# Kernel tuning notes

Measured on AMD Instinct MI355X. Metric: run time of the kernel, lower is better.

Reference implementation:

```python
import jax, jax.numpy as jnp
import numpy as np

HEADS = 16
DIM = 1024
D_K = DIM // HEADS
SEQ = 2048


def setup_inputs() -> dict:
    key = jax.random.key(0)
    ks = jax.random.split(key, 11)
    s = 1.0 / np.sqrt(DIM).astype(np.float32)
    return {
        "q": jax.random.normal(ks[0], (SEQ, DIM), jnp.float32),
        "k": jax.random.normal(ks[1], (SEQ, DIM), jnp.float32),
        "v": jax.random.normal(ks[2], (SEQ, DIM), jnp.float32),
        "Wq": jax.random.normal(ks[3], (DIM, DIM), jnp.float32) * s,
        "bq": jax.random.normal(ks[4], (DIM,), jnp.float32) * 0.01,
        "Wk": jax.random.normal(ks[5], (DIM, DIM), jnp.float32) * s,
        "bk": jax.random.normal(ks[6], (DIM,), jnp.float32) * 0.01,
        "Wv": jax.random.normal(ks[7], (DIM, DIM), jnp.float32) * s,
        "bv": jax.random.normal(ks[8], (DIM,), jnp.float32) * 0.01,
        "Wo": jax.random.normal(ks[9], (DIM, DIM), jnp.float32) * s,
        "bo": jax.random.normal(ks[10], (DIM,), jnp.float32) * 0.01,
    }


def reference(q, k, v, Wq, bq, Wk, bk, Wv, bv, Wo, bo):
    S = q.shape[0]
    # torch Linear: x @ W.T + b; view to (1, S, H, d_k) then transpose to (1, H, S, d_k)
    def proj(x, W, b):
        return (x @ W.T + b).reshape(1, S, HEADS, D_K).transpose(0, 2, 1, 3)

    qh = proj(q, Wq, bq)  # (1, H, S, d)
    kh = proj(k, Wk, bk)
    vh = proj(v, Wv, bv)

    scale = 1.0 / np.sqrt(D_K).astype(np.float32)
    scores = jnp.einsum("bhqd,bhkd->bhqk", qh, kh) * scale  # (1, H, S, S)
    # NOTE: source applies softmax over dim=1 == the HEADS axis (faithful quirk)
    attn = jax.nn.softmax(scores, axis=1)
    ctx = jnp.einsum("bhqk,bhkd->bhqd", attn, vh)  # (1, H, S, d)
    concat = ctx.transpose(0, 2, 1, 3).reshape(1, S, DIM)
    return concat @ Wo.T + bo
```

## Files before the change

kernel.cpp:

```cpp
#include <hip/hip_runtime.h>
#include <hip/hip_fp16.h>


typedef _Float16 f16;
typedef _Float16 f16x4 __attribute__((ext_vector_type(4)));
typedef _Float16 f16x8 __attribute__((ext_vector_type(8)));
typedef float    f32x4 __attribute__((ext_vector_type(4)));

#define S_LEN 2048
#define DIM   1024
#define NH    16
#define DK    64
#define EXP2K 0.1803368801111244f

#define MFMA(a, b, c) __builtin_amdgcn_mfma_f32_16x16x32_f16(a, b, c, 0, 0, 0)

#define VM_WAIT0   asm volatile("s_waitcnt vmcnt(0)" ::: "memory")
#define WG_BARRIER asm volatile("s_barrier" ::: "memory")

typedef __attribute__((address_space(1))) void g_void;
typedef __attribute__((address_space(3))) void l_void;

static __device__ __forceinline__ void gload_lds16(const void* g, void* l) {
  __builtin_amdgcn_global_load_lds((g_void*)g, (l_void*)l, 16, 0, 0);
}

static __device__ __forceinline__ float exp_s(float s) {
  return __builtin_amdgcn_exp2f(s * EXP2K);
}

__global__ __launch_bounds__(256) void cvt_all(
    const float* __restrict__ q, const float* __restrict__ k, const float* __restrict__ v,
    const float* __restrict__ Wq, const float* __restrict__ Wk, const float* __restrict__ Wv,
    const float* __restrict__ Wo, f16* __restrict__ qh, f16* __restrict__ kh,
    f16* __restrict__ vh, f16* __restrict__ wqh, f16* __restrict__ wkh,
    f16* __restrict__ wvh, f16* __restrict__ woh) {
  const size_t M = 1048576;
  const int seg = blockIdx.y;
  const float* src;
  f16* dst;
  switch (seg) {
    case 0: src = q;      dst = qh;      break;
    case 1: src = q + M;  dst = qh + M;  break;
    case 2: src = k;      dst = kh;      break;
    case 3: src = k + M;  dst = kh + M;  break;
    case 4: src = v;      dst = vh;      break;
    case 5: src = v + M;  dst = vh + M;  break;
    case 6: src = Wq;     dst = wqh;     break;
    case 7: src = Wk;     dst = wkh;     break;
    case 8: src = Wv;     dst = wvh;     break;
    default: src = Wo;    dst = woh;     break;
  }
  int i = blockIdx.x * 256 + threadIdx.x;
  float4 vv = ((const float4*)src)[i];
  f16x4 o = {(f16)vv.x, (f16)vv.y, (f16)vv.z, (f16)vv.w};
  ((f16x4*)dst)[i] = o;
}

__global__ __launch_bounds__(256) void sum_halves(const f16* __restrict__ a,
                                                  const f16* __restrict__ b,
                                                  f16* __restrict__ o) {
  int i = blockIdx.x * 256 + threadIdx.x;
  f16x8 x = ((const f16x8*)a)[i];
  f16x8 y = ((const f16x8*)b)[i];
  f16x8 r;
#pragma unroll
  for (int j = 0; j < 8; j++) r[j] = (f16)((float)x[j] + (float)y[j]);
  ((f16x8*)o)[i] = r;
}

static __device__ __forceinline__ void gemm32_core(const f16* __restrict__ X,
                                                   const f16* __restrict__ W,
                                                   int k0, int k1, int bm, int bn,
                                                   f16* As, f16* Bs,
                                                   f32x4 (&acc)[4][2]) {
  const int tid = threadIdx.x;
  const int wv = tid >> 6;
  const int lane = tid & 63;
  const int qd = lane >> 4;
  const int l16 = lane & 15;
  const int wm = (wv & 1) * 64;
  const int wn = (wv >> 1) * 32;
  const int lr4 = lane >> 2, lc4 = lane & 3;

  const f16* gA = X + (size_t)(bm + wv * 32 + lr4) * DIM + k0 + lc4 * 8;
  const f16* gB = W + (size_t)(bn + wv * 16 + lr4) * DIM + k0 + lc4 * 8;
  const int np = (k1 - k0) >> 5;

  gload_lds16(gA, As + (wv * 32) * 32);
  gload_lds16(gA + 16 * DIM, As + (wv * 32 + 16) * 32);
  gload_lds16(gB, Bs + (wv * 16) * 32);

#pragma unroll 2
  for (int t = 0; t < np; t++) {
    const int buf = t & 1;
    VM_WAIT0;
    WG_BARRIER;
    if (t + 1 < np) {
      const f16* gA1 = gA + (t + 1) * 32;
      const f16* gB1 = gB + (t + 1) * 32;
      f16* dA = As + (buf ^ 1) * (128 * 32);
      f16* dB = Bs + (buf ^ 1) * (64 * 32);
      gload_lds16(gA1, dA + (wv * 32) * 32);
      gload_lds16(gA1 + 16 * DIM, dA + (wv * 32 + 16) * 32);
      gload_lds16(gB1, dB + (wv * 16) * 32);
    }
    const f16* A = As + buf * (128 * 32);
    const f16* B = Bs + buf * (64 * 32);
    f16x8 bf[2];
#pragma unroll
    for (int ni = 0; ni < 2; ni++)
      bf[ni] = *(const f16x8*)&B[(wn + ni * 16 + l16) * 32 + qd * 8];
#pragma unroll
    for (int mi = 0; mi < 4; mi++) {
      f16x8 af = *(const f16x8*)&A[(wm + mi * 16 + l16) * 32 + qd * 8];
#pragma unroll
      for (int ni = 0; ni < 2; ni++)
        acc[mi][ni] = MFMA(af, bf[ni], acc[mi][ni]);
    }
  }
}

__global__ __launch_bounds__(256) void gemm_qkv(
    const f16* __restrict__ X0, const f16* __restrict__ X1, const f16* __restrict__ X2,
    const f16* __restrict__ W0, const f16* __restrict__ W1, const f16* __restrict__ W2,
    const float* __restrict__ b0, const float* __restrict__ b1, const float* __restrict__ b2,
    f16* __restrict__ o0, f16* __restrict__ o1, f16* __restrict__ o2) {
  __shared__ __align__(16) f16 As[2 * 128 * 32];
  __shared__ __align__(16) f16 Bs[2 * 64 * 32];
  const int z = blockIdx.z;
  const f16* X = z == 0 ? X0 : z == 1 ? X1 : X2;
  const f16* W = z == 0 ? W0 : z == 1 ? W1 : W2;
  const float* bias = z == 0 ? b0 : z == 1 ? b1 : b2;
  f16* outh = z == 0 ? o0 : z == 1 ? o1 : o2;

  const int bm = blockIdx.y * 128, bn = blockIdx.x * 64;
  f32x4 acc[4][2];
#pragma unroll
  for (int a = 0; a < 4; a++)
#pragma unroll
    for (int b = 0; b < 2; b++) acc[a][b] = (f32x4){0.f, 0.f, 0.f, 0.f};

  gemm32_core(X, W, 0, DIM, bm, bn, As, Bs, acc);

  const int tid = threadIdx.x;
  const int wv = tid >> 6, lane = tid & 63;
  const int qd = lane >> 4, l16 = lane & 15;
  const int wm = (wv & 1) * 64, wn = (wv >> 1) * 32;
#pragma unroll
  for (int mi = 0; mi < 4; mi++) {
#pragma unroll
    for (int ni = 0; ni < 2; ni++) {
      const int gm = bm + wm + mi * 16 + qd * 4;
      const int gn = bn + wn + ni * 16 + l16;
      const float bs = bias[gn];
      if (z == 2) {
        f16x4 o = {(f16)(acc[mi][ni][0] + bs), (f16)(acc[mi][ni][1] + bs),
                   (f16)(acc[mi][ni][2] + bs), (f16)(acc[mi][ni][3] + bs)};
        const int pj = (gm & ~31) + ((gm >> 2) & 3) * 8 + ((gm >> 4) & 1) * 4;
        *(f16x4*)&outh[(size_t)gn * S_LEN + pj] = o;
      } else {
#pragma unroll
        for (int r = 0; r < 4; r++)
          outh[(size_t)(gm + r) * DIM + gn] = (f16)(acc[mi][ni][r] + bs);
      }
    }
  }
}

__global__ __launch_bounds__(256) void gemm_out(const f16* __restrict__ X,
                                                const f16* __restrict__ W,
                                                const float* __restrict__ bias,
                                                float* __restrict__ outf) {
  __shared__ __align__(16) f16 As[2 * 64 * 32];
  __shared__ __align__(16) f16 Bs[2 * 64 * 32];
  const int tid = threadIdx.x;
  const int wv = tid >> 6;
  const int lane = tid & 63;
  const int qd = lane >> 4;
  const int l16 = lane & 15;
  const int wm = (wv & 1) * 32;
  const int wn = (wv >> 1) * 32;
  const int lr4 = lane >> 2, lc4 = lane & 3;
  const int bm = blockIdx.y * 64, bn = blockIdx.x * 64;

  const f16* gA = X + (size_t)(bm + wv * 16 + lr4) * DIM + lc4 * 8;
  const f16* gB = W + (size_t)(bn + wv * 16 + lr4) * DIM + lc4 * 8;

  f32x4 acc[2][2];
#pragma unroll
  for (int a = 0; a < 2; a++)
#pragma unroll
    for (int b = 0; b < 2; b++) acc[a][b] = (f32x4){0.f, 0.f, 0.f, 0.f};

  gload_lds16(gA, As + (wv * 16) * 32);
  gload_lds16(gB, Bs + (wv * 16) * 32);

#pragma unroll 2
  for (int t = 0; t < 32; t++) {
    const int buf = t & 1;
    VM_WAIT0;
    WG_BARRIER;
    if (t + 1 < 32) {
      gload_lds16(gA + (t + 1) * 32, As + (buf ^ 1) * (64 * 32) + (wv * 16) * 32);
      gload_lds16(gB + (t + 1) * 32, Bs + (buf ^ 1) * (64 * 32) + (wv * 16) * 32);
    }
    const f16* A = As + buf * (64 * 32);
    const f16* B = Bs + buf * (64 * 32);
    f16x8 bf[2];
#pragma unroll
    for (int ni = 0; ni < 2; ni++)
      bf[ni] = *(const f16x8*)&B[(wn + ni * 16 + l16) * 32 + qd * 8];
#pragma unroll
    for (int mi = 0; mi < 2; mi++) {
      f16x8 af = *(const f16x8*)&A[(wm + mi * 16 + l16) * 32 + qd * 8];
#pragma unroll
      for (int ni = 0; ni < 2; ni++)
        acc[mi][ni] = MFMA(af, bf[ni], acc[mi][ni]);
    }
  }

#pragma unroll
  for (int mi = 0; mi < 2; mi++) {
#pragma unroll
    for (int ni = 0; ni < 2; ni++) {
      const int gm = bm + wm + mi * 16 + qd * 4;
      const int gn = bn + wn + ni * 16 + l16;
      const float bs = bias[gn];
#pragma unroll
      for (int r = 0; r < 4; r++)
        outf[(size_t)(gm + r) * DIM + gn] = acc[mi][ni][r] + bs;
    }
  }
}

__global__ __launch_bounds__(256) void attn_denom(const f16* __restrict__ Qp,
                                                  const f16* __restrict__ Kp,
                                                  f16* __restrict__ IDn) {
  __shared__ __align__(16) f16 Qs[2][2][64 * 32];
  __shared__ __align__(16) f16 Ks[2][2][64 * 32];
  const int tid = threadIdx.x;
  const int wv = tid >> 6;
  const int lane = tid & 63;
  const int qd = lane >> 4;
  const int l16 = lane & 15;
  const int wm = (wv & 1) * 32, wn = (wv >> 1) * 32;
  const int bi = blockIdx.y * 64, bj = blockIdx.x * 64;
  const int lr4 = lane >> 2, lc4 = lane & 3;
  const int kkw = wv & 1;
  const int q0 = (wv >> 1) * 2;
  const int ssw = (lc4 ^ ((lr4 >> 1) & 3)) * 8;
  const int rsw = (qd ^ ((l16 >> 1) & 3)) * 8;

  f32x4 dsum[2][2];
#pragma unroll
  for (int a = 0; a < 2; a++)
#pragma unroll
    for (int b = 0; b < 2; b++) dsum[a][b] = (f32x4){0.f, 0.f, 0.f, 0.f};

  {
    const f16* gq = Qp + (size_t)(bi + q0 * 16 + lr4) * DIM + kkw * 32 + ssw;
    const f16* gk = Kp + (size_t)(bj + q0 * 16 + lr4) * DIM + kkw * 32 + ssw;
#pragma unroll
    for (int t = 0; t < 2; t++) {
      gload_lds16(gq + (size_t)t * 16 * DIM, &Qs[0][kkw][(q0 + t) * 16 * 32]);
      gload_lds16(gk + (size_t)t * 16 * DIM, &Ks[0][kkw][(q0 + t) * 16 * 32]);
    }
  }

#pragma unroll 2
  for (int h = 0; h < NH; h++) {
    const int buf = h & 1;
    VM_WAIT0;
    WG_BARRIER;
    if (h + 1 < NH) {
      const f16* gq = Qp + (size_t)(bi + q0 * 16 + lr4) * DIM + (h + 1) * DK + kkw * 32 + ssw;
      const f16* gk = Kp + (size_t)(bj + q0 * 16 + lr4) * DIM + (h + 1) * DK + kkw * 32 + ssw;
#pragma unroll
      for (int t = 0; t < 2; t++) {
        gload_lds16(gq + (size_t)t * 16 * DIM, &Qs[buf ^ 1][kkw][(q0 + t) * 16 * 32]);
        gload_lds16(gk + (size_t)t * 16 * DIM, &Ks[buf ^ 1][kkw][(q0 + t) * 16 * 32]);
      }
    }

#pragma unroll
    for (int mi = 0; mi < 2; mi++) {
      f16x8 af0 = *(const f16x8*)&Qs[buf][0][(wm + mi * 16 + l16) * 32 + rsw];
      f16x8 af1 = *(const f16x8*)&Qs[buf][1][(wm + mi * 16 + l16) * 32 + rsw];
#pragma unroll
      for (int ni = 0; ni < 2; ni++) {
        f16x8 bf0 = *(const f16x8*)&Ks[buf][0][(wn + ni * 16 + l16) * 32 + rsw];
        f16x8 bf1 = *(const f16x8*)&Ks[buf][1][(wn + ni * 16 + l16) * 32 + rsw];
        f32x4 s = {0.f, 0.f, 0.f, 0.f};
        s = MFMA(af0, bf0, s);
        s = MFMA(af1, bf1, s);
#pragma unroll
        for (int r = 0; r < 4; r++) dsum[mi][ni][r] += exp_s(s[r]);
      }
    }
  }
#pragma unroll
  for (int mi = 0; mi < 2; mi++)
#pragma unroll
    for (int ni = 0; ni < 2; ni++)
#pragma unroll
      for (int r = 0; r < 4; r++) {
        const int gi = bi + wm + mi * 16 + qd * 4 + r;
        const int gj = bj + wn + ni * 16 + l16;
        const int pj = (gj & ~31) + ((gj >> 2) & 3) * 8 + ((gj >> 4) & 1) * 4 + (gj & 3);
        IDn[(size_t)gi * S_LEN + pj] = (f16)(1.f / dsum[mi][ni][r]);
      }
}

__global__ __launch_bounds__(256, 8) void attn_ctx(const f16* __restrict__ Qp,
                                                   const f16* __restrict__ Kp,
                                                   const f16* __restrict__ Vt,
                                                   const f16* __restrict__ IDn,
                                                   f16* __restrict__ C0,
                                                   f16* __restrict__ C1) {
  __shared__ __align__(16) f16 Ks[2][2][32 * 32];
  __shared__ __align__(16) f16 Vs[2][64 * 32];
  const int tid = threadIdx.x;
  const int wv = tid >> 6;
  const int lane = tid & 63;
  const int qd = lane >> 4;
  const int l16 = lane & 15;
  const int flat = blockIdx.x + (blockIdx.y << 5) + (blockIdx.z << 9);
  const int nf = ((flat & 7) << 7) + (flat >> 3);
  const int h = (nf >> 5) & 15;
  const int iw = (nf & 31) * 64 + wv * 16;
  const int z = nf >> 9;
  const int jb = z * 1024;
  f16* Cz = z == 0 ? C0 : C1;
  const int lr4 = lane >> 2, lc4 = lane & 3;
  const int kkw = wv & 1;
  const int rhw = wv >> 1;
  const int ssw = (lc4 ^ ((lr4 >> 1) & 3)) * 8;
  const int rsw = (qd ^ ((l16 >> 1) & 3)) * 8;

  f16x8 aq[2];
#pragma unroll
  for (int kk = 0; kk < 2; kk++)
    aq[kk] = *(const f16x8*)(Qp + (size_t)(iw + l16) * DIM + h * DK + kk * 32 + qd * 8);

  f32x4 acc[4];
#pragma unroll
  for (int b = 0; b < 4; b++) acc[b] = (f32x4){0.f, 0.f, 0.f, 0.f};

  f16x8 idn[2];

  auto issue = [&](int tt, int pb) {
    const int j1 = jb + tt * 32;
    gload_lds16(Kp + (size_t)(j1 + rhw * 16 + lr4) * DIM + h * DK + kkw * 32 + ssw,
                &Ks[pb][kkw][(rhw * 16) * 32]);
    gload_lds16(Vt + (size_t)(h * DK + wv * 16 + lr4) * S_LEN + j1 + ssw,
                &Vs[pb][(wv * 16) * 32]);
    idn[pb] = *(const f16x8*)(IDn + (size_t)(iw + l16) * S_LEN + j1 + qd * 8);
  };

  issue(0, 0);

#pragma unroll 2
  for (int t = 0; t < 32; t++) {
    const int buf = t & 1;
    VM_WAIT0;
    WG_BARRIER;
    if (t + 1 < 32) issue(t + 1, buf ^ 1);

    f16x8 bk[2][2];
#pragma unroll
    for (int ni = 0; ni < 2; ni++)
#pragma unroll
      for (int kk = 0; kk < 2; kk++)
        bk[ni][kk] = *(const f16x8*)&Ks[buf][kk][(ni * 16 + l16) * 32 + rsw];

    f32x4 st0 = {0.f, 0.f, 0.f, 0.f};
    f32x4 st1 = {0.f, 0.f, 0.f, 0.f};
    st0 = MFMA(bk[0][0], aq[0], st0);
    st0 = MFMA(bk[0][1], aq[1], st0);
    st1 = MFMA(bk[1][0], aq[0], st1);
    st1 = MFMA(bk[1][1], aq[1], st1);
    f16x8 p;
#pragma unroll
    for (int r = 0; r < 4; r++) p[r] = (f16)(exp_s(st0[r]) * (float)idn[buf][r]);
#pragma unroll
    for (int r = 0; r < 4; r++) p[4 + r] = (f16)(exp_s(st1[r]) * (float)idn[buf][4 + r]);

    f16x8 bv[4];
#pragma unroll
    for (int nd = 0; nd < 4; nd++)
      bv[nd] = *(const f16x8*)&Vs[buf][(nd * 16 + l16) * 32 + rsw];
#pragma unroll
    for (int nd = 0; nd < 4; nd++)
      acc[nd] = MFMA(p, bv[nd], acc[nd]);
  }

#pragma unroll
  for (int nd = 0; nd < 4; nd++)
#pragma unroll
    for (int r = 0; r < 4; r++)
      Cz[(size_t)(iw + qd * 4 + r) * DIM + h * DK + nd * 16 + l16] = (f16)acc[nd][r];
}

extern "C" void kernel_launch(void* const* d_in, const int* in_sizes, int n_in,
                              void* d_out, int out_size, void* d_ws, size_t ws_size,
                              hipStream_t stream) {
  const float* q  = (const float*)d_in[0];
  const float* k  = (const float*)d_in[1];
  const float* v  = (const float*)d_in[2];
  const float* Wq = (const float*)d_in[3];
  const float* bq = (const float*)d_in[4];
  const float* Wk = (const float*)d_in[5];
  const float* bk = (const float*)d_in[6];
  const float* Wv = (const float*)d_in[7];
  const float* bv = (const float*)d_in[8];
  const float* Wo = (const float*)d_in[9];
  const float* bo = (const float*)d_in[10];
  float* out = (float*)d_out;

  f16* w = (f16*)d_ws;
  f16* qh  = w;
  f16* kh  = qh + (size_t)S_LEN * DIM;
  f16* vh  = kh + (size_t)S_LEN * DIM;
  f16* wqh = vh + (size_t)S_LEN * DIM;
  f16* wkh = wqh + (size_t)DIM * DIM;
  f16* wvh = wkh + (size_t)DIM * DIM;
  f16* woh = wvh + (size_t)DIM * DIM;
  f16* Qp  = woh + (size_t)DIM * DIM;
  f16* Kp  = Qp + (size_t)S_LEN * DIM;
  f16* Vt  = Kp + (size_t)S_LEN * DIM;
  f16* IDn = qh;
  f16* C0  = vh;
  f16* C1  = wqh;
  f16* Ct  = qh;

  dim3 b256(256);
  cvt_all<<<dim3(1024, 10), b256, 0, stream>>>(q, k, v, Wq, Wk, Wv, Wo,
                                               qh, kh, vh, wqh, wkh, wvh, woh);

  gemm_qkv<<<dim3(DIM / 64, S_LEN / 128, 3), b256, 0, stream>>>(
      qh, kh, vh, wqh, wkh, wvh, bq, bk, bv, Qp, Kp, Vt);

  attn_denom<<<dim3(S_LEN / 64, S_LEN / 64), b256, 0, stream>>>(Qp, Kp, IDn);
  attn_ctx<<<dim3(S_LEN / 64, NH, 2), b256, 0, stream>>>(Qp, Kp, Vt, IDn, C0, C1);

  const int n8 = S_LEN * DIM / 8;
  sum_halves<<<n8 / 256, b256, 0, stream>>>(C0, C1, Ct);

  gemm_out<<<dim3(DIM / 64, S_LEN / 64), b256, 0, stream>>>(Ct, woh, bo, out);
}
```

Baseline: 209.2 us.

## Double attn_ctx key tile to 64 per iteration and swizzle attn_denom block order

```diff
diff --git a/kernel.cpp b/kernel.cpp
--- a/kernel.cpp
+++ b/kernel.cpp
@@ -245,7 +245,9 @@
   const int qd = lane >> 4;
   const int l16 = lane & 15;
   const int wm = (wv & 1) * 32, wn = (wv >> 1) * 32;
-  const int bi = blockIdx.y * 64, bj = blockIdx.x * 64;
+  const int flat = blockIdx.x + (blockIdx.y << 5);
+  const int nf = ((flat & 7) << 7) + (flat >> 3);
+  const int bi = (nf >> 5) * 64, bj = (nf & 31) * 64;
   const int lr4 = lane >> 2, lc4 = lane & 3;
   const int kkw = wv & 1;
   const int q0 = (wv >> 1) * 2;
@@ -312,14 +314,14 @@
       }
 }
 
-__global__ __launch_bounds__(256, 8) void attn_ctx(const f16* __restrict__ Qp,
+__global__ __launch_bounds__(256, 4) void attn_ctx(const f16* __restrict__ Qp,
                                                    const f16* __restrict__ Kp,
                                                    const f16* __restrict__ Vt,
                                                    const f16* __restrict__ IDn,
                                                    f16* __restrict__ C0,
                                                    f16* __restrict__ C1) {
-  __shared__ __align__(16) f16 Ks[2][2][32 * 32];
-  __shared__ __align__(16) f16 Vs[2][64 * 32];
+  __shared__ __align__(16) f16 Ks[2][2][64 * 32];
+  __shared__ __align__(16) f16 Vs[2][64 * 64];
   const int tid = threadIdx.x;
   const int wv = tid >> 6;
   const int lane = tid & 63;
@@ -333,10 +335,12 @@
   const int jb = z * 1024;
   f16* Cz = z == 0 ? C0 : C1;
   const int lr4 = lane >> 2, lc4 = lane & 3;
+  const int lr8 = lane >> 3, lc8 = lane & 7;
   const int kkw = wv & 1;
   const int rhw = wv >> 1;
   const int ssw = (lc4 ^ ((lr4 >> 1) & 3)) * 8;
   const int rsw = (qd ^ ((l16 >> 1) & 3)) * 8;
+  const int l7 = l16 & 7;
 
   f16x8 aq[2];
 #pragma unroll
@@ -347,52 +351,62 @@
 #pragma unroll
   for (int b = 0; b < 4; b++) acc[b] = (f32x4){0.f, 0.f, 0.f, 0.f};
 
-  f16x8 idn[2];
+  f16x8 idn[2][2];
 
   auto issue = [&](int tt, int pb) {
-    const int j1 = jb + tt * 32;
-    gload_lds16(Kp + (size_t)(j1 + rhw * 16 + lr4) * DIM + h * DK + kkw * 32 + ssw,
-                &Ks[pb][kkw][(rhw * 16) * 32]);
-    gload_lds16(Vt + (size_t)(h * DK + wv * 16 + lr4) * S_LEN + j1 + ssw,
-                &Vs[pb][(wv * 16) * 32]);
-    idn[pb] = *(const f16x8*)(IDn + (size_t)(iw + l16) * S_LEN + j1 + qd * 8);
+    const int j1 = jb + tt * 64;
+    const f16* gk = Kp + (size_t)(j1 + rhw * 16 + lr4) * DIM + h * DK + kkw * 32 + ssw;
+    gload_lds16(gk, &Ks[pb][kkw][(rhw * 16) * 32]);
+    gload_lds16(gk + (size_t)32 * DIM, &Ks[pb][kkw][(rhw * 16 + 32) * 32]);
+    const f16* gv = Vt + (size_t)(h * DK + wv * 16 + lr8) * S_LEN + j1 + (lc8 ^ lr8) * 8;
+    gload_lds16(gv, &Vs[pb][(wv * 16) * 64]);
+    gload_lds16(gv + (size_t)8 * S_LEN, &Vs[pb][(wv * 16 + 8) * 64]);
+#pragma unroll
+    for (int js = 0; js < 2; js++)
+      idn[pb][js] = *(const f16x8*)(IDn + (size_t)(iw + l16) * S_LEN + j1 + js * 32 + qd * 8);
   };
 
   issue(0, 0);
 
 #pragma unroll 2
-  for (int t = 0; t < 32; t++) {
+  for (int t = 0; t < 16; t++) {
     const int buf = t & 1;
     VM_WAIT0;
     WG_BARRIER;
-    if (t + 1 < 32) issue(t + 1, buf ^ 1);
-
-    f16x8 bk[2][2];
-#pragma unroll
-    for (int ni = 0; ni < 2; ni++)
-#pragma unroll
-      for (int kk = 0; kk < 2; kk++)
-        bk[ni][kk] = *(const f16x8*)&Ks[buf][kk][(ni * 16 + l16) * 32 + rsw];
-
-    f32x4 st0 = {0.f, 0.f, 0.f, 0.f};
-    f32x4 st1 = {0.f, 0.f, 0.f, 0.f};
-    st0 = MFMA(bk[0][0], aq[0], st0);
-    st0 = MFMA(bk[0][1], aq[1], st0);
-    st1 = MFMA(bk[1][0], aq[0], st1);
-    st1 = MFMA(bk[1][1], aq[1], st1);
-    f16x8 p;
-#pragma unroll
-    for (int r = 0; r < 4; r++) p[r] = (f16)(exp_s(st0[r]) * (float)idn[buf][r]);
-#pragma unroll
-    for (int r = 0; r < 4; r++) p[4 + r] = (f16)(exp_s(st1[r]) * (float)idn[buf][4 + r]);
-
-    f16x8 bv[4];
-#pragma unroll
-    for (int nd = 0; nd < 4; nd++)
-      bv[nd] = *(const f16x8*)&Vs[buf][(nd * 16 + l16) * 32 + rsw];
-#pragma unroll
-    for (int nd = 0; nd < 4; nd++)
-      acc[nd] = MFMA(p, bv[nd], acc[nd]);
+    if (t + 1 < 16) issue(t + 1, buf ^ 1);
+
+    f16x8 pa[2];
+#pragma unroll
+    for (int js = 0; js < 2; js++) {
+      f16x8 bk0[2], bk1[2];
+#pragma unroll
+      for (int kk = 0; kk < 2; kk++) {
+        bk0[kk] = *(const f16x8*)&Ks[buf][kk][((js * 2) * 16 + l16) * 32 + rsw];
+        bk1[kk] = *(const f16x8*)&Ks[buf][kk][((js * 2 + 1) * 16 + l16) * 32 + rsw];
+      }
+      f32x4 st0 = {0.f, 0.f, 0.f, 0.f};
+      f32x4 st1 = {0.f, 0.f, 0.f, 0.f};
+      st0 = MFMA(bk0[0], aq[0], st0);
+      st0 = MFMA(bk0[1], aq[1], st0);
+      st1 = MFMA(bk1[0], aq[0], st1);
+      st1 = MFMA(bk1[1], aq[1], st1);
+      f16x8 p;
+#pragma unroll
+      for (int r = 0; r < 4; r++) p[r] = (f16)(exp_s(st0[r]) * (float)idn[buf][js][r]);
+#pragma unroll
+      for (int r = 0; r < 4; r++) p[4 + r] = (f16)(exp_s(st1[r]) * (float)idn[buf][js][4 + r]);
+      pa[js] = p;
+    }
+
+#pragma unroll
+    for (int js = 0; js < 2; js++) {
+#pragma unroll
+      for (int nd = 0; nd < 4; nd++) {
+        f16x8 bv = *(const f16x8*)&Vs[buf][(nd * 16 + l16) * 64 +
+                                          (((js * 4 + qd) ^ l7) * 8)];
+        acc[nd] = MFMA(pa[js], bv, acc[nd]);
+      }
+    }
   }
 
 #pragma unroll
```

Result: no change. 205.2 us (-1.9%).
